# Kernel optimization log

Measured on AMD Instinct MI355X. Metric: run time of the kernel, lower is better.

The kernel has to match this reference:

```python
import jax, jax.numpy as jnp
import numpy as np

NUM_HEADS = 16
WINDOW = 32
HIDDEN = 1024
HEAD_DIM = HIDDEN // NUM_HEADS


def setup_inputs() -> dict:
    key = jax.random.key(0)
    ks = jax.random.split(key, 9)
    B, S, H = 2, 2048, HIDDEN
    s = 0.02
    return {
        "hidden_states": jax.random.normal(ks[0], (B, S, H), jnp.float32),
        "Wq": jax.random.normal(ks[1], (H, H), jnp.float32) * s,
        "bq": jnp.zeros((H,), jnp.float32),
        "Wk": jax.random.normal(ks[2], (H, H), jnp.float32) * s,
        "bk": jnp.zeros((H,), jnp.float32),
        "Wv": jax.random.normal(ks[3], (H, H), jnp.float32) * s,
        "bv": jnp.zeros((H,), jnp.float32),
        "Wo": jax.random.normal(ks[4], (H, H), jnp.float32) * s,
        "bo": jnp.zeros((H,), jnp.float32),
    }


def reference(hidden_states, Wq, bq, Wk, bk, Wv, bv, Wo, bo):
    B, S, H = hidden_states.shape
    scale = jnp.sqrt(jnp.asarray(HEAD_DIM, hidden_states.dtype))
    # torch Linear: x @ W.T + b
    q = (hidden_states @ Wq.T + bq).reshape(B, S, NUM_HEADS, HEAD_DIM)
    k = (hidden_states @ Wk.T + bk).reshape(B, S, NUM_HEADS, HEAD_DIM)
    v = (hidden_states @ Wv.T + bv).reshape(B, S, NUM_HEADS, HEAD_DIM)
    # Full scores; block-causal pattern: query in block bi sees keys in blocks <= bi.
    scores = jnp.einsum("bihd,bjhd->bhij", q, k) / scale  # [B,H,S,S]
    blk = jnp.arange(S) // WINDOW
    allowed = blk[:, None] >= blk[None, :]  # [S,S]
    # Faithful to original: unfilled (future-block) entries are ZERO, not -inf,
    # and still participate in the softmax.
    scores = jnp.where(allowed, scores, jnp.zeros((), scores.dtype))
    probs = jax.nn.softmax(scores, axis=-1)
    ctx = jnp.einsum("bhij,bjhd->bihd", probs, v).reshape(B, S, H)
    return ctx @ Wo.T + bo
```

## Files before the change

### kernel.cpp

```cpp
#include <hip/hip_runtime.h>
#include <cstdint>

namespace {

constexpr int kS   = 2048;
constexpr int kNH  = 16;
constexpr int kHD  = 64;
constexpr int kH   = 1024;
constexpr int kB   = 2;
constexpr int kWin = 32;
constexpr int kNBlk = kS / kWin;
constexpr float kQScale = 0.18033688011112042f;

typedef __attribute__((ext_vector_type(8))) short short8v;
typedef __attribute__((ext_vector_type(4))) float f32x4;
typedef __attribute__((ext_vector_type(4))) unsigned short u16x4;
typedef __attribute__((ext_vector_type(8))) unsigned short u16x8;
typedef __attribute__((ext_vector_type(2))) unsigned int u32x2;

static __device__ __forceinline__ unsigned short f2bf(float f) {
  unsigned int u = __float_as_uint(f);
  return (unsigned short)((u + 0x7fffu + ((u >> 16) & 1u)) >> 16);
}
static __device__ __forceinline__ float bf2f(unsigned short b) {
  return __uint_as_float((unsigned int)b << 16);
}
static __device__ __forceinline__ void async16(const void* g, void* l) {
  __builtin_amdgcn_global_load_lds((__attribute__((address_space(1))) void*)(g),
                                   (__attribute__((address_space(3))) void*)(l),
                                   16, 0, 0);
}

__global__ __launch_bounds__(256) void cvt_bf16(
    const float* __restrict__ hs, const float* __restrict__ Wq,
    const float* __restrict__ Wk, const float* __restrict__ Wv,
    const float* __restrict__ Wo, unsigned short* __restrict__ out)
{
  const size_t idx = ((size_t)blockIdx.x * 256 + threadIdx.x) * 8;
  const int seg = (int)(idx >> 20);
  const size_t off = idx & ((1u << 20) - 1);
  const float* src;
  if (seg < 4)       src = hs + idx;
  else if (seg == 4) src = Wq + off;
  else if (seg == 5) src = Wk + off;
  else if (seg == 6) src = Wv + off;
  else               src = Wo + off;
  const float4 f0 = *(const float4*)(src);
  const float4 f1 = *(const float4*)(src + 4);
  u16x8 pk;
  pk[0] = f2bf(f0.x); pk[1] = f2bf(f0.y); pk[2] = f2bf(f0.z); pk[3] = f2bf(f0.w);
  pk[4] = f2bf(f1.x); pk[5] = f2bf(f1.y); pk[6] = f2bf(f1.z); pk[7] = f2bf(f1.w);
  *(u16x8*)(out + idx) = pk;
}

template <int MT, int EPI>
__global__ __launch_bounds__(256) void gemm_mfma(
    const unsigned short* __restrict__ A, const unsigned short* __restrict__ W,
    const float* __restrict__ b0, const float* __restrict__ b1,
    const float* __restrict__ b2, float* __restrict__ Cf,
    unsigned short* __restrict__ Dq, unsigned short* __restrict__ Dk,
    unsigned short* __restrict__ Dv, int M, int N, int K)
{
  constexpr int BMr = MT * 32;
  constexpr int AG  = MT / 2;
  __shared__ unsigned short As[BMr * 32];
  __shared__ unsigned short Ws[128 * 32];
  const int tid  = threadIdx.x;
  const int wave = tid >> 6, lane = tid & 63;
  const int q16  = lane & 15, quad = lane >> 4;
  const int wm   = wave & 1,  wn   = wave >> 1;
  const int bm = blockIdx.y * BMr, bn = blockIdx.x * 128;

  const int lrow   = lane >> 2;
  const int lchunk = (lane & 3) ^ ((lane >> 3) & 3);

  const unsigned short* gA[AG];
  unsigned short* lA[AG];
#pragma unroll
  for (int g = 0; g < AG; ++g) {
    gA[g] = A + (size_t)(bm + wave * 16 * AG + g * 16 + lrow) * K + lchunk * 8;
    lA[g] = As + (wave * 16 * AG + g * 16) * 32;
  }
  const unsigned short* gW0 = W + (size_t)(bn + wave * 32 + lrow) * K + lchunk * 8;
  const unsigned short* gW1 = gW0 + (size_t)16 * K;
  unsigned short* lW0 = Ws + (wave * 32) * 32;
  unsigned short* lW1 = lW0 + 16 * 32;

  const int swz = quad ^ ((q16 >> 1) & 3);
  const unsigned short* fA = As + (wm * (MT * 16) + q16) * 32 + swz * 8;
  const unsigned short* fB = Ws + (wn * 64 + q16) * 32 + swz * 8;

  const f32x4 zero = {0.f, 0.f, 0.f, 0.f};
  f32x4 acc[MT][4];
#pragma unroll
  for (int i = 0; i < MT; ++i)
#pragma unroll
    for (int j = 0; j < 4; ++j) acc[i][j] = zero;

  for (int k0 = 0; k0 < K; k0 += 32) {
    __syncthreads();
#pragma unroll
    for (int g = 0; g < AG; ++g) { async16(gA[g], lA[g]); gA[g] += 32; }
    async16(gW0, lW0);
    async16(gW1, lW1);
    gW0 += 32; gW1 += 32;
    __syncthreads();

    short8v a[MT], b[4];
#pragma unroll
    for (int t = 0; t < MT; ++t) a[t] = *(const short8v*)(fA + t * 16 * 32);
#pragma unroll
    for (int t = 0; t < 4; ++t)  b[t] = *(const short8v*)(fB + t * 16 * 32);
#pragma unroll
    for (int mt = 0; mt < MT; ++mt)
#pragma unroll
      for (int nt = 0; nt < 4; ++nt)
        acc[mt][nt] = __builtin_amdgcn_mfma_f32_16x16x32_bf16(a[mt], b[nt], acc[mt][nt], 0, 0, 0);
  }

#pragma unroll
  for (int nt = 0; nt < 4; ++nt) {
    const int col = bn + wn * 64 + nt * 16 + q16;
#pragma unroll
    for (int mt = 0; mt < MT; ++mt) {
      const int row0 = bm + wm * (MT * 16) + mt * 16 + quad * 4;
      const f32x4 av = acc[mt][nt];
      if (EPI == 0) {
        const float bv = b0[col];
#pragma unroll
        for (int r = 0; r < 4; ++r)
          Cf[(size_t)(row0 + r) * N + col] = av[r] + bv;
      } else {
        const int mat = col >> 10, c = col & 1023;
        const int b = row0 >> 11, s0 = row0 & 2047;
        const int h = c >> 6, d = c & 63;
        const size_t bhslot = (size_t)(b * kNH + h);
        if (mat == 0) {
          const float bv = b0[c];
          unsigned short* base = Dq + ((bhslot * kS + s0) * kHD + d);
#pragma unroll
          for (int r = 0; r < 4; ++r) base[(size_t)r * kHD] = f2bf((av[r] + bv) * kQScale);
        } else if (mat == 1) {
          const float bv = b1[c];
          unsigned short* base = Dk + ((bhslot * kS + s0) * kHD + d);
#pragma unroll
          for (int r = 0; r < 4; ++r) base[(size_t)r * kHD] = f2bf(av[r] + bv);
        } else {
          const float bv = b2[c];
          u16x4 pk;
          pk[0] = f2bf(av[0] + bv); pk[1] = f2bf(av[1] + bv);
          pk[2] = f2bf(av[2] + bv); pk[3] = f2bf(av[3] + bv);
          *(u16x4*)(Dv + (bhslot * kHD + d) * kS + s0) = pk;
        }
      }
    }
  }
}

__global__ __launch_bounds__(256) void vprefix_kernel(
    const unsigned short* __restrict__ vt, float* __restrict__ vrest)
{
  __shared__ float bsum[64][64];
  __shared__ float ptot[4][64];
  const int bh = blockIdx.x;
  const int d = threadIdx.x & 63, part = threadIdx.x >> 6;
  const unsigned short* base = vt + ((size_t)bh * kHD + d) * kS;
#pragma unroll 4
  for (int j = 0; j < 16; ++j) {
    const int jb = part * 16 + j;
    const unsigned short* p = base + jb * kWin;
    float s = 0.f;
#pragma unroll
    for (int i = 0; i < 4; ++i) {
      const u16x8 v = *(const u16x8*)(p + i * 8);
#pragma unroll
      for (int e = 0; e < 8; ++e) s += bf2f(v[e]);
    }
    bsum[jb][d] = s;
  }
  __syncthreads();
  float t = 0.f;
#pragma unroll
  for (int j = 0; j < 16; ++j) t += bsum[part * 16 + j][d];
  ptot[part][d] = t;
  __syncthreads();
  float s = 0.f;
  for (int p2 = part + 1; p2 < 4; ++p2) s += ptot[p2][d];
#pragma unroll
  for (int j = 15; j >= 0; --j) {
    const int bi = part * 16 + j;
    vrest[((size_t)bh * kNBlk + bi) * kHD + d] = s;
    s += bsum[bi][d];
  }
}

__global__ __launch_bounds__(256, 4) void attn_mfma(
    const unsigned short* __restrict__ qb, const unsigned short* __restrict__ kb,
    const unsigned short* __restrict__ vtb, const float* __restrict__ vrest,
    unsigned short* __restrict__ ctx)
{
  __shared__ union SM {
    unsigned short es[4][1024];
    struct { float part[2][2048]; float den[4][32]; } m;
  } sm;

  const int tid  = threadIdx.x;
  const int wave = tid >> 6;
  const int lane = tid & 63;
  const int q16  = lane & 15;
  const int quad = lane >> 4;
  const int bh = blockIdx.x & 31;
  const int bi = (kNBlk - 1) - (blockIdx.x >> 5);
  const int b  = bh >> 4, h = bh & 15;

  const unsigned short* Qb  = qb  + ((size_t)bh * kS + (size_t)bi * kWin) * kHD;
  const unsigned short* Kb  = kb  + (size_t)bh * kS * kHD;
  const unsigned short* Vtb = vtb + (size_t)bh * kHD * kS;

  short8v qf[2][2];
#pragma unroll
  for (int qt = 0; qt < 2; ++qt)
#pragma unroll
    for (int ks = 0; ks < 2; ++ks)
      qf[qt][ks] = *(const short8v*)(Qb + (qt * 16 + q16) * kHD + ks * 32 + quad * 8);

  short8v ones;
#pragma unroll
  for (int i = 0; i < 8; ++i) ones[i] = (q16 == 0) ? (short)0x3F80 : (short)0;

  const f32x4 zero = {0.f, 0.f, 0.f, 0.f};
  f32x4 acc[2][4];
#pragma unroll
  for (int mt = 0; mt < 2; ++mt)
#pragma unroll
    for (int nt = 0; nt < 4; ++nt) acc[mt][nt] = zero;
  f32x4 accd[2] = {zero, zero};

  unsigned short* esw = sm.es[wave];
  const int swz = (q16 >> 2) & 3;

  for (int jb = wave; jb <= bi; jb += 4) {
    const unsigned short* Kj = Kb + (size_t)jb * kWin * kHD;
    short8v kf[2][2];
#pragma unroll
    for (int kt = 0; kt < 2; ++kt)
#pragma unroll
      for (int ks = 0; ks < 2; ++ks)
        kf[kt][ks] = *(const short8v*)(Kj + (kt * 16 + q16) * kHD + ks * 32 + quad * 8);
    short8v vf[4];
#pragma unroll
    for (int nt = 0; nt < 4; ++nt)
      vf[nt] = *(const short8v*)(Vtb + (size_t)(nt * 16 + q16) * kS + jb * kWin + quad * 8);

    f32x4 st[2][2];
#pragma unroll
    for (int kt = 0; kt < 2; ++kt)
#pragma unroll
      for (int qt = 0; qt < 2; ++qt) {
        f32x4 c = zero;
        c = __builtin_amdgcn_mfma_f32_16x16x32_bf16(kf[kt][0], qf[qt][0], c, 0, 0, 0);
        c = __builtin_amdgcn_mfma_f32_16x16x32_bf16(kf[kt][1], qf[qt][1], c, 0, 0, 0);
        st[kt][qt] = c;
      }

#pragma unroll
    for (int kt = 0; kt < 2; ++kt) {
      const int g = kt * 2 + (quad >> 1);
      const int col = ((g ^ swz) * 8) + (quad & 1) * 4;
#pragma unroll
      for (int qt = 0; qt < 2; ++qt) {
        const unsigned int r0 = __float_as_uint(__builtin_amdgcn_exp2f(st[kt][qt][0])) + 0x8000u;
        const unsigned int r1 = __float_as_uint(__builtin_amdgcn_exp2f(st[kt][qt][1])) + 0x8000u;
        const unsigned int r2 = __float_as_uint(__builtin_amdgcn_exp2f(st[kt][qt][2])) + 0x8000u;
        const unsigned int r3 = __float_as_uint(__builtin_amdgcn_exp2f(st[kt][qt][3])) + 0x8000u;
        u32x2 w;
        w[0] = __builtin_amdgcn_perm(r1, r0, 0x07060302u);
        w[1] = __builtin_amdgcn_perm(r3, r2, 0x07060302u);
        *(u32x2*)(esw + (qt * 16 + q16) * 32 + col) = w;
      }
    }

    const short8v af0 = *(const short8v*)(esw + (q16)      * 32 + (quad ^ swz) * 8);
    const short8v af1 = *(const short8v*)(esw + (16 + q16) * 32 + (quad ^ swz) * 8);

#pragma unroll
    for (int nt = 0; nt < 4; ++nt) {
      acc[0][nt] = __builtin_amdgcn_mfma_f32_16x16x32_bf16(af0, vf[nt], acc[0][nt], 0, 0, 0);
      acc[1][nt] = __builtin_amdgcn_mfma_f32_16x16x32_bf16(af1, vf[nt], acc[1][nt], 0, 0, 0);
    }
    accd[0] = __builtin_amdgcn_mfma_f32_16x16x32_bf16(af0, ones, accd[0], 0, 0, 0);
    accd[1] = __builtin_amdgcn_mfma_f32_16x16x32_bf16(af1, ones, accd[1], 0, 0, 0);
  }

  __syncthreads();
  if (q16 == 0) {
#pragma unroll
    for (int mt = 0; mt < 2; ++mt)
#pragma unroll
      for (int r = 0; r < 4; ++r)
        sm.m.den[wave][mt * 16 + quad * 4 + r] = accd[mt][r];
  }
  if (wave < 2) {
    float* p = sm.m.part[wave];
#pragma unroll
    for (int mt = 0; mt < 2; ++mt)
#pragma unroll
      for (int nt = 0; nt < 4; ++nt)
#pragma unroll
        for (int r = 0; r < 4; ++r)
          p[((mt * 4 + nt) * 4 + r) * 64 + lane] = acc[mt][nt][r];
  }
  __syncthreads();
  if (wave >= 2) {
    float* p = sm.m.part[wave - 2];
#pragma unroll
    for (int mt = 0; mt < 2; ++mt)
#pragma unroll
      for (int nt = 0; nt < 4; ++nt)
#pragma unroll
        for (int r = 0; r < 4; ++r)
          p[((mt * 4 + nt) * 4 + r) * 64 + lane] += acc[mt][nt][r];
  }
  __syncthreads();

  {
    const int nt = wave;
    const int dim = nt * 16 + q16;
    const float vr = vrest[((size_t)bh * kNBlk + bi) * kHD + dim];
    const float nrest = 32.0f * (float)((kNBlk - 1) - bi);
    unsigned short* outb = ctx + ((size_t)b * kS + (size_t)bi * kWin) * kH + h * kHD;
#pragma unroll
    for (int mt = 0; mt < 2; ++mt) {
#pragma unroll
      for (int r = 0; r < 4; ++r) {
        const int idx = ((mt * 4 + nt) * 4 + r) * 64 + lane;
        const int qrow = mt * 16 + quad * 4 + r;
        const float den = sm.m.den[0][qrow] + sm.m.den[1][qrow] +
                          sm.m.den[2][qrow] + sm.m.den[3][qrow] + nrest;
        outb[(size_t)qrow * kH + dim] =
            f2bf((sm.m.part[0][idx] + sm.m.part[1][idx] + vr) / den);
      }
    }
  }
}

}

extern "C" void kernel_launch(void* const* d_in, const int* in_sizes, int n_in,
                              void* d_out, int out_size, void* d_ws, size_t ws_size,
                              hipStream_t stream) {
  const float* hs = (const float*)d_in[0];
  const float* Wq = (const float*)d_in[1];
  const float* bq = (const float*)d_in[2];
  const float* Wk = (const float*)d_in[3];
  const float* bk = (const float*)d_in[4];
  const float* Wv = (const float*)d_in[5];
  const float* bv = (const float*)d_in[6];
  const float* Wo = (const float*)d_in[7];
  const float* bo = (const float*)d_in[8];

  char* wsb = (char*)d_ws;
  unsigned short* hsb   = (unsigned short*)(wsb);
  unsigned short* wqkv  = hsb + (4u << 20);
  unsigned short* wob   = hsb + (7u << 20);
  unsigned short* qbuf  = (unsigned short*)(wsb + (16u << 20));
  unsigned short* kbuf  = (unsigned short*)(wsb + (24u << 20));
  unsigned short* vtbuf = (unsigned short*)(wsb + (32u << 20));
  unsigned short* ctxb  = (unsigned short*)(wsb + (40u << 20));
  float*          vrest = (float*)         (wsb + (48u << 20));

  const int M = kB * kS;

  cvt_bf16<<<4096, 256, 0, stream>>>(hs, Wq, Wk, Wv, Wo, hsb);
  gemm_mfma<4, 1><<<dim3(3072 / 128, M / 128), 256, 0, stream>>>(
      hsb, wqkv, bq, bk, bv, nullptr, qbuf, kbuf, vtbuf, M, 3072, kH);
  vprefix_kernel<<<kB * kNH, 256, 0, stream>>>(vtbuf, vrest);
  attn_mfma<<<kNBlk * kB * kNH, 256, 0, stream>>>(qbuf, kbuf, vtbuf, vrest, ctxb);
  gemm_mfma<2, 0><<<dim3(kH / 128, M / 64), 256, 0, stream>>>(
      ctxb, wob, bo, nullptr, nullptr, (float*)d_out, nullptr, nullptr, nullptr,
      M, kH, kH);
}
```

Before: 231.7 us.

## Software-pipeline attention loop with double-buffered K/V register prefetch

Restructures the per-wave key-block loop to handle two blocks per iteration. The K and V fragments for the next pair are prefetched into registers while the current pair's QK, exp and PV MFMAs run, and each block gets its own LDS staging buffer. The aim is to hide global-load latency behind compute. In exchange it doubles LDS staging and adds register pressure, which under launch_bounds(256,4) may cause spills. It also issues redundant loads of block `wave` when no next block exists.

```diff
diff --git a/kernel.cpp b/kernel.cpp
--- a/kernel.cpp
+++ b/kernel.cpp
@@ -194,13 +194,74 @@
   }
 }
 
+__device__ __forceinline__ void load_kf(short8v kf[2][2],
+    const unsigned short* __restrict__ Kb, int jb, int q16, int quad) {
+  const unsigned short* Kj = Kb + (size_t)jb * kWin * kHD;
+#pragma unroll
+  for (int kt = 0; kt < 2; ++kt)
+#pragma unroll
+    for (int ks = 0; ks < 2; ++ks)
+      kf[kt][ks] = *(const short8v*)(Kj + (kt * 16 + q16) * kHD + ks * 32 + quad * 8);
+}
+__device__ __forceinline__ void load_vf(short8v vf[4],
+    const unsigned short* __restrict__ Vtb, int jb, int q16, int quad) {
+#pragma unroll
+  for (int nt = 0; nt < 4; ++nt)
+    vf[nt] = *(const short8v*)(Vtb + (size_t)(nt * 16 + q16) * kS + jb * kWin + quad * 8);
+}
+__device__ __forceinline__ void qk_tiles(const short8v kf[2][2],
+    const short8v qf[2][2], f32x4 st[2][2]) {
+  const f32x4 zero = {0.f, 0.f, 0.f, 0.f};
+#pragma unroll
+  for (int kt = 0; kt < 2; ++kt)
+#pragma unroll
+    for (int qt = 0; qt < 2; ++qt) {
+      f32x4 c = zero;
+      c = __builtin_amdgcn_mfma_f32_16x16x32_bf16(kf[kt][0], qf[qt][0], c, 0, 0, 0);
+      c = __builtin_amdgcn_mfma_f32_16x16x32_bf16(kf[kt][1], qf[qt][1], c, 0, 0, 0);
+      st[kt][qt] = c;
+    }
+}
+__device__ __forceinline__ void exp_pack(const f32x4 st[2][2],
+    unsigned short* __restrict__ esw, int q16, int quad, int swz) {
+#pragma unroll
+  for (int kt = 0; kt < 2; ++kt) {
+    const int g = kt * 2 + (quad >> 1);
+    const int col = ((g ^ swz) * 8) + (quad & 1) * 4;
+#pragma unroll
+    for (int qt = 0; qt < 2; ++qt) {
+      const unsigned int r0 = __float_as_uint(__builtin_amdgcn_exp2f(st[kt][qt][0])) + 0x8000u;
+      const unsigned int r1 = __float_as_uint(__builtin_amdgcn_exp2f(st[kt][qt][1])) + 0x8000u;
+      const unsigned int r2 = __float_as_uint(__builtin_amdgcn_exp2f(st[kt][qt][2])) + 0x8000u;
+      const unsigned int r3 = __float_as_uint(__builtin_amdgcn_exp2f(st[kt][qt][3])) + 0x8000u;
+      u32x2 w;
+      w[0] = __builtin_amdgcn_perm(r1, r0, 0x07060302u);
+      w[1] = __builtin_amdgcn_perm(r3, r2, 0x07060302u);
+      *(u32x2*)(esw + (qt * 16 + q16) * 32 + col) = w;
+    }
+  }
+}
+__device__ __forceinline__ void ev_acc(const unsigned short* __restrict__ esw,
+    const short8v vf[4], const short8v& ones, int q16, int quad, int swz,
+    f32x4 acc[2][4], f32x4 accd[2]) {
+  const short8v af0 = *(const short8v*)(esw + (q16)      * 32 + (quad ^ swz) * 8);
+  const short8v af1 = *(const short8v*)(esw + (16 + q16) * 32 + (quad ^ swz) * 8);
+#pragma unroll
+  for (int nt = 0; nt < 4; ++nt) {
+    acc[0][nt] = __builtin_amdgcn_mfma_f32_16x16x32_bf16(af0, vf[nt], acc[0][nt], 0, 0, 0);
+    acc[1][nt] = __builtin_amdgcn_mfma_f32_16x16x32_bf16(af1, vf[nt], acc[1][nt], 0, 0, 0);
+  }
+  accd[0] = __builtin_amdgcn_mfma_f32_16x16x32_bf16(af0, ones, accd[0], 0, 0, 0);
+  accd[1] = __builtin_amdgcn_mfma_f32_16x16x32_bf16(af1, ones, accd[1], 0, 0, 0);
+}
+
 __global__ __launch_bounds__(256, 4) void attn_mfma(
     const unsigned short* __restrict__ qb, const unsigned short* __restrict__ kb,
     const unsigned short* __restrict__ vtb, const float* __restrict__ vrest,
     unsigned short* __restrict__ ctx)
 {
   __shared__ union SM {
-    unsigned short es[4][1024];
+    unsigned short es[4][2][1024];
     struct { float part[2][2048]; float den[4][32]; } m;
   } sm;
 
@@ -236,60 +297,37 @@
     for (int nt = 0; nt < 4; ++nt) acc[mt][nt] = zero;
   f32x4 accd[2] = {zero, zero};
 
-  unsigned short* esw = sm.es[wave];
+  unsigned short* esA = sm.es[wave][0];
+  unsigned short* esB = sm.es[wave][1];
   const int swz = (q16 >> 2) & 3;
 
-  for (int jb = wave; jb <= bi; jb += 4) {
-    const unsigned short* Kj = Kb + (size_t)jb * kWin * kHD;
-    short8v kf[2][2];
-#pragma unroll
-    for (int kt = 0; kt < 2; ++kt)
-#pragma unroll
-      for (int ks = 0; ks < 2; ++ks)
-        kf[kt][ks] = *(const short8v*)(Kj + (kt * 16 + q16) * kHD + ks * 32 + quad * 8);
-    short8v vf[4];
-#pragma unroll
-    for (int nt = 0; nt < 4; ++nt)
-      vf[nt] = *(const short8v*)(Vtb + (size_t)(nt * 16 + q16) * kS + jb * kWin + quad * 8);
-
-    f32x4 st[2][2];
-#pragma unroll
-    for (int kt = 0; kt < 2; ++kt)
-#pragma unroll
-      for (int qt = 0; qt < 2; ++qt) {
-        f32x4 c = zero;
-        c = __builtin_amdgcn_mfma_f32_16x16x32_bf16(kf[kt][0], qf[qt][0], c, 0, 0, 0);
-        c = __builtin_amdgcn_mfma_f32_16x16x32_bf16(kf[kt][1], qf[qt][1], c, 0, 0, 0);
-        st[kt][qt] = c;
-      }
-
-#pragma unroll
-    for (int kt = 0; kt < 2; ++kt) {
-      const int g = kt * 2 + (quad >> 1);
-      const int col = ((g ^ swz) * 8) + (quad & 1) * 4;
-#pragma unroll
-      for (int qt = 0; qt < 2; ++qt) {
-        const unsigned int r0 = __float_as_uint(__builtin_amdgcn_exp2f(st[kt][qt][0])) + 0x8000u;
-        const unsigned int r1 = __float_as_uint(__builtin_amdgcn_exp2f(st[kt][qt][1])) + 0x8000u;
-        const unsigned int r2 = __float_as_uint(__builtin_amdgcn_exp2f(st[kt][qt][2])) + 0x8000u;
-        const unsigned int r3 = __float_as_uint(__builtin_amdgcn_exp2f(st[kt][qt][3])) + 0x8000u;
-        u32x2 w;
-        w[0] = __builtin_amdgcn_perm(r1, r0, 0x07060302u);
-        w[1] = __builtin_amdgcn_perm(r3, r2, 0x07060302u);
-        *(u32x2*)(esw + (qt * 16 + q16) * 32 + col) = w;
-      }
-    }
-
-    const short8v af0 = *(const short8v*)(esw + (q16)      * 32 + (quad ^ swz) * 8);
-    const short8v af1 = *(const short8v*)(esw + (16 + q16) * 32 + (quad ^ swz) * 8);
-
-#pragma unroll
-    for (int nt = 0; nt < 4; ++nt) {
-      acc[0][nt] = __builtin_amdgcn_mfma_f32_16x16x32_bf16(af0, vf[nt], acc[0][nt], 0, 0, 0);
-      acc[1][nt] = __builtin_amdgcn_mfma_f32_16x16x32_bf16(af1, vf[nt], acc[1][nt], 0, 0, 0);
-    }
-    accd[0] = __builtin_amdgcn_mfma_f32_16x16x32_bf16(af0, ones, accd[0], 0, 0, 0);
-    accd[1] = __builtin_amdgcn_mfma_f32_16x16x32_bf16(af1, ones, accd[1], 0, 0, 0);
+  short8v kfA[2][2], vfA[4], kfB[2][2], vfB[4];
+  int jb = wave;
+  if (jb <= bi)     { load_kf(kfA, Kb, jb, q16, quad);     load_vf(vfA, Vtb, jb, q16, quad); }
+  if (jb + 4 <= bi) { load_kf(kfB, Kb, jb + 4, q16, quad); load_vf(vfB, Vtb, jb + 4, q16, quad); }
+
+  while (jb + 4 <= bi) {
+    const int na = (jb + 8  <= bi) ? jb + 8  : wave;
+    const int nb = (jb + 12 <= bi) ? jb + 12 : wave;
+    f32x4 stA[2][2];
+    qk_tiles(kfA, qf, stA);
+    load_kf(kfA, Kb, na, q16, quad);
+    exp_pack(stA, esA, q16, quad, swz);
+    f32x4 stB[2][2];
+    qk_tiles(kfB, qf, stB);
+    load_kf(kfB, Kb, nb, q16, quad);
+    exp_pack(stB, esB, q16, quad, swz);
+    ev_acc(esA, vfA, ones, q16, quad, swz, acc, accd);
+    load_vf(vfA, Vtb, na, q16, quad);
+    ev_acc(esB, vfB, ones, q16, quad, swz, acc, accd);
+    load_vf(vfB, Vtb, nb, q16, quad);
+    jb += 8;
+  }
+  if (jb <= bi) {
+    f32x4 stA[2][2];
+    qk_tiles(kfA, qf, stA);
+    exp_pack(stA, esA, q16, quad, swz);
+    ev_acc(esA, vfA, ones, q16, quad, swz, acc, accd);
   }
 
   __syncthreads();
```

After: 291.5 us. 25.8% more time.

## Process two query blocks per attention CTA and deepen GEMM K-tile to 64

Applied to the files above, without the earlier changes.

Each attention block now handles two adjacent 32-row query windows (64 queries), so every K/V tile loaded from memory is reused across twice as many queries and the grid is halved. The row-sum denominator is now accumulated in VALU from the exp values with a cross-lane shuffle, replacing the extra MFMA against a ones vector. Separately, the shared GEMM kernel stages 64-wide K slices with an 8-chunk XOR swizzle, which halves the number of barrier pairs per tile. The cost is more registers and LDS per CTA (launch bounds lowered to 3 waves per SIMD), fewer attention CTAs, and a tail iteration for the upper block that runs on a single wave.

```diff
diff --git a/kernel.cpp b/kernel.cpp
--- a/kernel.cpp
+++ b/kernel.cpp
@@ -62,33 +62,39 @@
     unsigned short* __restrict__ Dv, int M, int N, int K)
 {
   constexpr int BMr = MT * 32;
-  constexpr int AG  = MT / 2;
-  __shared__ unsigned short As[BMr * 32];
-  __shared__ unsigned short Ws[128 * 32];
+  __shared__ unsigned short As[BMr * 64];
+  __shared__ unsigned short Ws[128 * 64];
   const int tid  = threadIdx.x;
   const int wave = tid >> 6, lane = tid & 63;
   const int q16  = lane & 15, quad = lane >> 4;
   const int wm   = wave & 1,  wn   = wave >> 1;
   const int bm = blockIdx.y * BMr, bn = blockIdx.x * 128;
 
-  const int lrow   = lane >> 2;
-  const int lchunk = (lane & 3) ^ ((lane >> 3) & 3);
-
-  const unsigned short* gA[AG];
-  unsigned short* lA[AG];
-#pragma unroll
-  for (int g = 0; g < AG; ++g) {
-    gA[g] = A + (size_t)(bm + wave * 16 * AG + g * 16 + lrow) * K + lchunk * 8;
-    lA[g] = As + (wave * 16 * AG + g * 16) * 32;
-  }
-  const unsigned short* gW0 = W + (size_t)(bn + wave * 32 + lrow) * K + lchunk * 8;
-  const unsigned short* gW1 = gW0 + (size_t)16 * K;
-  unsigned short* lW0 = Ws + (wave * 32) * 32;
-  unsigned short* lW1 = lW0 + 16 * 32;
-
-  const int swz = quad ^ ((q16 >> 1) & 3);
-  const unsigned short* fA = As + (wm * (MT * 16) + q16) * 32 + swz * 8;
-  const unsigned short* fB = Ws + (wn * 64 + q16) * 32 + swz * 8;
+  const int lrow8 = lane >> 3;
+  const int lch   = lane & 7;
+  const int gch   = lch ^ lrow8;
+
+  const unsigned short* gA[MT];
+  unsigned short* lA[MT];
+#pragma unroll
+  for (int g = 0; g < MT; ++g) {
+    const int row0 = wave * MT * 8 + g * 8;
+    gA[g] = A + (size_t)(bm + row0 + lrow8) * K + gch * 8;
+    lA[g] = As + row0 * 64;
+  }
+  const unsigned short* gW[4];
+  unsigned short* lW[4];
+#pragma unroll
+  for (int g = 0; g < 4; ++g) {
+    const int row0 = wave * 32 + g * 8;
+    gW[g] = W + (size_t)(bn + row0 + lrow8) * K + gch * 8;
+    lW[g] = Ws + row0 * 64;
+  }
+
+  const unsigned short* fA = As + (wm * (MT * 16) + q16) * 64;
+  const unsigned short* fB = Ws + (wn * 64 + q16) * 64;
+  const int sl0 = ((quad)     ^ (q16 & 7)) * 8;
+  const int sl1 = ((quad + 4) ^ (q16 & 7)) * 8;
 
   const f32x4 zero = {0.f, 0.f, 0.f, 0.f};
   f32x4 acc[MT][4];
@@ -97,20 +103,28 @@
 #pragma unroll
     for (int j = 0; j < 4; ++j) acc[i][j] = zero;
 
-  for (int k0 = 0; k0 < K; k0 += 32) {
+  for (int k0 = 0; k0 < K; k0 += 64) {
     __syncthreads();
 #pragma unroll
-    for (int g = 0; g < AG; ++g) { async16(gA[g], lA[g]); gA[g] += 32; }
-    async16(gW0, lW0);
-    async16(gW1, lW1);
-    gW0 += 32; gW1 += 32;
+    for (int g = 0; g < MT; ++g) { async16(gA[g], lA[g]); gA[g] += 64; }
+#pragma unroll
+    for (int g = 0; g < 4; ++g)  { async16(gW[g], lW[g]); gW[g] += 64; }
     __syncthreads();
 
     short8v a[MT], b[4];
 #pragma unroll
-    for (int t = 0; t < MT; ++t) a[t] = *(const short8v*)(fA + t * 16 * 32);
-#pragma unroll
-    for (int t = 0; t < 4; ++t)  b[t] = *(const short8v*)(fB + t * 16 * 32);
+    for (int t = 0; t < MT; ++t) a[t] = *(const short8v*)(fA + t * 16 * 64 + sl0);
+#pragma unroll
+    for (int t = 0; t < 4; ++t)  b[t] = *(const short8v*)(fB + t * 16 * 64 + sl0);
+#pragma unroll
+    for (int mt = 0; mt < MT; ++mt)
+#pragma unroll
+      for (int nt = 0; nt < 4; ++nt)
+        acc[mt][nt] = __builtin_amdgcn_mfma_f32_16x16x32_bf16(a[mt], b[nt], acc[mt][nt], 0, 0, 0);
+#pragma unroll
+    for (int t = 0; t < MT; ++t) a[t] = *(const short8v*)(fA + t * 16 * 64 + sl1);
+#pragma unroll
+    for (int t = 0; t < 4; ++t)  b[t] = *(const short8v*)(fB + t * 16 * 64 + sl1);
 #pragma unroll
     for (int mt = 0; mt < MT; ++mt)
 #pragma unroll
@@ -194,14 +208,72 @@
   }
 }
 
-__global__ __launch_bounds__(256, 4) void attn_mfma(
+template <int QT0>
+__device__ __forceinline__ void attn_iter(
+    const unsigned short* __restrict__ Kb, const unsigned short* __restrict__ Vtb,
+    int jb, const short8v qf[4][2], unsigned short* __restrict__ esw,
+    int q16, int quad, int swz, f32x4 acc[4][4], float dAcc[4])
+{
+  const unsigned short* Kj = Kb + (size_t)jb * kWin * kHD;
+  short8v kf[2][2];
+#pragma unroll
+  for (int kt = 0; kt < 2; ++kt)
+#pragma unroll
+    for (int ks = 0; ks < 2; ++ks)
+      kf[kt][ks] = *(const short8v*)(Kj + (kt * 16 + q16) * kHD + ks * 32 + quad * 8);
+
+  const f32x4 zero = {0.f, 0.f, 0.f, 0.f};
+#pragma unroll
+  for (int kt = 0; kt < 2; ++kt) {
+    f32x4 st[4];
+#pragma unroll
+    for (int qt = QT0; qt < 4; ++qt) {
+      f32x4 c = zero;
+      c = __builtin_amdgcn_mfma_f32_16x16x32_bf16(kf[kt][0], qf[qt][0], c, 0, 0, 0);
+      c = __builtin_amdgcn_mfma_f32_16x16x32_bf16(kf[kt][1], qf[qt][1], c, 0, 0, 0);
+      st[qt] = c;
+    }
+    const int g = kt * 2 + (quad >> 1);
+    const int col = ((g ^ swz) * 8) + (quad & 1) * 4;
+#pragma unroll
+    for (int qt = QT0; qt < 4; ++qt) {
+      const float e0 = __builtin_amdgcn_exp2f(st[qt][0]);
+      const float e1 = __builtin_amdgcn_exp2f(st[qt][1]);
+      const float e2 = __builtin_amdgcn_exp2f(st[qt][2]);
+      const float e3 = __builtin_amdgcn_exp2f(st[qt][3]);
+      dAcc[qt] += (e0 + e1) + (e2 + e3);
+      const unsigned int r0 = __float_as_uint(e0) + 0x8000u;
+      const unsigned int r1 = __float_as_uint(e1) + 0x8000u;
+      const unsigned int r2 = __float_as_uint(e2) + 0x8000u;
+      const unsigned int r3 = __float_as_uint(e3) + 0x8000u;
+      u32x2 w;
+      w[0] = __builtin_amdgcn_perm(r1, r0, 0x07060302u);
+      w[1] = __builtin_amdgcn_perm(r3, r2, 0x07060302u);
+      *(u32x2*)(esw + (qt * 16 + q16) * 32 + col) = w;
+    }
+  }
+  short8v af[4];
+#pragma unroll
+  for (int mt = QT0; mt < 4; ++mt)
+    af[mt] = *(const short8v*)(esw + (mt * 16 + q16) * 32 + (quad ^ swz) * 8);
+#pragma unroll
+  for (int nt = 0; nt < 4; ++nt) {
+    const short8v vfv = *(const short8v*)(Vtb + (size_t)(nt * 16 + q16) * kS +
+                                          jb * kWin + quad * 8);
+#pragma unroll
+    for (int mt = QT0; mt < 4; ++mt)
+      acc[mt][nt] = __builtin_amdgcn_mfma_f32_16x16x32_bf16(af[mt], vfv, acc[mt][nt], 0, 0, 0);
+  }
+}
+
+__global__ __launch_bounds__(256, 3) void attn_mfma(
     const unsigned short* __restrict__ qb, const unsigned short* __restrict__ kb,
     const unsigned short* __restrict__ vtb, const float* __restrict__ vrest,
     unsigned short* __restrict__ ctx)
 {
   __shared__ union SM {
-    unsigned short es[4][1024];
-    struct { float part[2][2048]; float den[4][32]; } m;
+    unsigned short es[4][2048];
+    struct { float part[2][4096]; float den[4][64]; } m;
   } sm;
 
   const int tid  = threadIdx.x;
@@ -210,100 +282,52 @@
   const int q16  = lane & 15;
   const int quad = lane >> 4;
   const int bh = blockIdx.x & 31;
-  const int bi = (kNBlk - 1) - (blockIdx.x >> 5);
+  const int pr = 31 - (blockIdx.x >> 5);
+  const int bilo = pr * 2, bihi = pr * 2 + 1;
   const int b  = bh >> 4, h = bh & 15;
 
-  const unsigned short* Qb  = qb  + ((size_t)bh * kS + (size_t)bi * kWin) * kHD;
+  const unsigned short* Qb  = qb  + ((size_t)bh * kS + (size_t)pr * 64) * kHD;
   const unsigned short* Kb  = kb  + (size_t)bh * kS * kHD;
   const unsigned short* Vtb = vtb + (size_t)bh * kHD * kS;
 
-  short8v qf[2][2];
-#pragma unroll
-  for (int qt = 0; qt < 2; ++qt)
+  short8v qf[4][2];
+#pragma unroll
+  for (int qt = 0; qt < 4; ++qt)
 #pragma unroll
     for (int ks = 0; ks < 2; ++ks)
       qf[qt][ks] = *(const short8v*)(Qb + (qt * 16 + q16) * kHD + ks * 32 + quad * 8);
 
-  short8v ones;
-#pragma unroll
-  for (int i = 0; i < 8; ++i) ones[i] = (q16 == 0) ? (short)0x3F80 : (short)0;
-
   const f32x4 zero = {0.f, 0.f, 0.f, 0.f};
-  f32x4 acc[2][4];
-#pragma unroll
-  for (int mt = 0; mt < 2; ++mt)
+  f32x4 acc[4][4];
+#pragma unroll
+  for (int mt = 0; mt < 4; ++mt)
 #pragma unroll
     for (int nt = 0; nt < 4; ++nt) acc[mt][nt] = zero;
-  f32x4 accd[2] = {zero, zero};
+  float dAcc[4] = {0.f, 0.f, 0.f, 0.f};
 
   unsigned short* esw = sm.es[wave];
   const int swz = (q16 >> 2) & 3;
 
-  for (int jb = wave; jb <= bi; jb += 4) {
-    const unsigned short* Kj = Kb + (size_t)jb * kWin * kHD;
-    short8v kf[2][2];
-#pragma unroll
-    for (int kt = 0; kt < 2; ++kt)
-#pragma unroll
-      for (int ks = 0; ks < 2; ++ks)
-        kf[kt][ks] = *(const short8v*)(Kj + (kt * 16 + q16) * kHD + ks * 32 + quad * 8);
-    short8v vf[4];
-#pragma unroll
-    for (int nt = 0; nt < 4; ++nt)
-      vf[nt] = *(const short8v*)(Vtb + (size_t)(nt * 16 + q16) * kS + jb * kWin + quad * 8);
-
-    f32x4 st[2][2];
-#pragma unroll
-    for (int kt = 0; kt < 2; ++kt)
-#pragma unroll
-      for (int qt = 0; qt < 2; ++qt) {
-        f32x4 c = zero;
-        c = __builtin_amdgcn_mfma_f32_16x16x32_bf16(kf[kt][0], qf[qt][0], c, 0, 0, 0);
-        c = __builtin_amdgcn_mfma_f32_16x16x32_bf16(kf[kt][1], qf[qt][1], c, 0, 0, 0);
-        st[kt][qt] = c;
-      }
-
-#pragma unroll
-    for (int kt = 0; kt < 2; ++kt) {
-      const int g = kt * 2 + (quad >> 1);
-      const int col = ((g ^ swz) * 8) + (quad & 1) * 4;
-#pragma unroll
-      for (int qt = 0; qt < 2; ++qt) {
-        const unsigned int r0 = __float_as_uint(__builtin_amdgcn_exp2f(st[kt][qt][0])) + 0x8000u;
-        const unsigned int r1 = __float_as_uint(__builtin_amdgcn_exp2f(st[kt][qt][1])) + 0x8000u;
-        const unsigned int r2 = __float_as_uint(__builtin_amdgcn_exp2f(st[kt][qt][2])) + 0x8000u;
-        const unsigned int r3 = __float_as_uint(__builtin_amdgcn_exp2f(st[kt][qt][3])) + 0x8000u;
-        u32x2 w;
-        w[0] = __builtin_amdgcn_perm(r1, r0, 0x07060302u);
-        w[1] = __builtin_amdgcn_perm(r3, r2, 0x07060302u);
-        *(u32x2*)(esw + (qt * 16 + q16) * 32 + col) = w;
-      }
-    }
-
-    const short8v af0 = *(const short8v*)(esw + (q16)      * 32 + (quad ^ swz) * 8);
-    const short8v af1 = *(const short8v*)(esw + (16 + q16) * 32 + (quad ^ swz) * 8);
-
-#pragma unroll
-    for (int nt = 0; nt < 4; ++nt) {
-      acc[0][nt] = __builtin_amdgcn_mfma_f32_16x16x32_bf16(af0, vf[nt], acc[0][nt], 0, 0, 0);
-      acc[1][nt] = __builtin_amdgcn_mfma_f32_16x16x32_bf16(af1, vf[nt], acc[1][nt], 0, 0, 0);
-    }
-    accd[0] = __builtin_amdgcn_mfma_f32_16x16x32_bf16(af0, ones, accd[0], 0, 0, 0);
-    accd[1] = __builtin_amdgcn_mfma_f32_16x16x32_bf16(af1, ones, accd[1], 0, 0, 0);
+  for (int jb = wave; jb <= bilo; jb += 4)
+    attn_iter<0>(Kb, Vtb, jb, qf, esw, q16, quad, swz, acc, dAcc);
+  if ((bihi & 3) == wave)
+    attn_iter<2>(Kb, Vtb, bihi, qf, esw, q16, quad, swz, acc, dAcc);
+
+#pragma unroll
+  for (int qt = 0; qt < 4; ++qt) {
+    dAcc[qt] += __shfl_xor(dAcc[qt], 16);
+    dAcc[qt] += __shfl_xor(dAcc[qt], 32);
   }
 
   __syncthreads();
-  if (q16 == 0) {
-#pragma unroll
-    for (int mt = 0; mt < 2; ++mt)
-#pragma unroll
-      for (int r = 0; r < 4; ++r)
-        sm.m.den[wave][mt * 16 + quad * 4 + r] = accd[mt][r];
+  if (quad == 0) {
+#pragma unroll
+    for (int qt = 0; qt < 4; ++qt) sm.m.den[wave][qt * 16 + q16] = dAcc[qt];
   }
   if (wave < 2) {
     float* p = sm.m.part[wave];
 #pragma unroll
-    for (int mt = 0; mt < 2; ++mt)
+    for (int mt = 0; mt < 4; ++mt)
 #pragma unroll
       for (int nt = 0; nt < 4; ++nt)
 #pragma unroll
@@ -314,7 +338,7 @@
   if (wave >= 2) {
     float* p = sm.m.part[wave - 2];
 #pragma unroll
-    for (int mt = 0; mt < 2; ++mt)
+    for (int mt = 0; mt < 4; ++mt)
 #pragma unroll
       for (int nt = 0; nt < 4; ++nt)
 #pragma unroll
@@ -326,17 +350,21 @@
   {
     const int nt = wave;
     const int dim = nt * 16 + q16;
-    const float vr = vrest[((size_t)bh * kNBlk + bi) * kHD + dim];
-    const float nrest = 32.0f * (float)((kNBlk - 1) - bi);
-    unsigned short* outb = ctx + ((size_t)b * kS + (size_t)bi * kWin) * kH + h * kHD;
-#pragma unroll
-    for (int mt = 0; mt < 2; ++mt) {
+    const float vrlo = vrest[((size_t)bh * kNBlk + bilo) * kHD + dim];
+    const float vrhi = vrest[((size_t)bh * kNBlk + bihi) * kHD + dim];
+    const float nrlo = 32.0f * (float)((kNBlk - 1) - bilo);
+    const float nrhi = 32.0f * (float)((kNBlk - 1) - bihi);
+    unsigned short* outb = ctx + ((size_t)b * kS + (size_t)pr * 64) * kH + h * kHD;
+#pragma unroll
+    for (int mt = 0; mt < 4; ++mt) {
+      const float vr = (mt < 2) ? vrlo : vrhi;
+      const float nr = (mt < 2) ? nrlo : nrhi;
 #pragma unroll
       for (int r = 0; r < 4; ++r) {
         const int idx = ((mt * 4 + nt) * 4 + r) * 64 + lane;
         const int qrow = mt * 16 + quad * 4 + r;
         const float den = sm.m.den[0][qrow] + sm.m.den[1][qrow] +
-                          sm.m.den[2][qrow] + sm.m.den[3][qrow] + nrest;
+                          sm.m.den[2][qrow] + sm.m.den[3][qrow] + nr;
         outb[(size_t)qrow * kH + dim] =
             f2bf((sm.m.part[0][idx] + sm.m.part[1][idx] + vr) / den);
       }
@@ -375,7 +403,7 @@
   gemm_mfma<4, 1><<<dim3(3072 / 128, M / 128), 256, 0, stream>>>(
       hsb, wqkv, bq, bk, bv, nullptr, qbuf, kbuf, vtbuf, M, 3072, kH);
   vprefix_kernel<<<kB * kNH, 256, 0, stream>>>(vtbuf, vrest);
-  attn_mfma<<<kNBlk * kB * kNH, 256, 0, stream>>>(qbuf, kbuf, vtbuf, vrest, ctxb);
+  attn_mfma<<<(kNBlk / 2) * kB * kNH, 256, 0, stream>>>(qbuf, kbuf, vtbuf, vrest, ctxb);
   gemm_mfma<2, 0><<<dim3(kH / 128, M / 64), 256, 0, stream>>>(
       ctxb, wob, bo, nullptr, nullptr, (float*)d_out, nullptr, nullptr, nullptr,
       M, kH, kH);
```

After: 201.8 us. 12.9% less time.
